# Kernel optimization log

Hardware: AMD Instinct MI355X
Metric: run time of the kernel (lower is better)

The kernel has to match this reference:

```python
import jax, jax.numpy as jnp
import numpy as np

V, D, L, S = 32000, 512, 4096, 256
LOG2 = float(np.log(2.0))


def _self_conflict(a, span):
    # a: [S, l] bool. Sequential: a[i] = a[i] & ~a[i-1] (using updated values).
    def step1(prev, cur):
        out = cur & ~prev
        return out, out
    first = a[:, 0]
    _, rest = jax.lax.scan(step1, first, a[:, 1:].T)  # scan over token axis
    a = jnp.concatenate([first[:, None], rest.T], axis=1)
    if span == 3:
        # second pass: a[i] = a[i] & ~a[i-2] on the updated array
        def step2(carry, cur):
            pm2, pm1 = carry
            out = cur & ~pm2
            return (pm1, out), out
        _, rest2 = jax.lax.scan(step2, (a[:, 0], a[:, 1]), a[:, 2:].T)
        a = jnp.concatenate([a[:, :2], rest2.T], axis=1)
    return a


def _shift_into(a1, off, L2):
    # hit[j] |= a1[j - off], zeros elsewhere
    B, l1 = a1.shape
    out = jnp.zeros((B, L2), dtype=bool)
    if off >= 0:
        end = min(L2, off + l1)
        return out.at[:, off:end].set(a1[:, :end - off])
    return out.at[:, :l1 + off].set(a1[:, -off:])


def _intersec_conflict(a1, a2, flag=False):
    # a2[j] cleared if any overlapping a1 span is active (set of shifts)
    l1, l2 = a1.shape[1], a2.shape[1]
    hit = jnp.zeros_like(a2)
    for i in range(l2 - l1 + 1):
        hit = hit | _shift_into(a1, i, l2)
    if flag:
        hit = hit | _shift_into(a1, -1, l2) | _shift_into(a1, 2, l2)
    return a2 & ~hit


def _forward(x, embd, w1, b1, w2, b2, w3, b3, g1, g2, g3, align1, align2, align3):
    emb = embd[x]                                   # [1, L, D]
    s2 = (emb[:, 1:] + emb[:, :-1]) / 2             # [1, L-1, D]
    s3 = (emb[:, 2:] + emb[:, 1:-1] + emb[:, :-2]) / 3
    heads = ((emb, w1, b1, g1, align1), (s2, w2, b2, g2, align2), (s3, w3, b3, g3, align3))
    stats, bools = [], []
    for spans, w, b, g, amask in heads:
        logits = spans @ w + b                      # [1, l, 2]
        logp = jax.nn.log_softmax(logits, axis=-1)
        p = jnp.exp(logp)
        nent = -(p * logp).sum(-1) / LOG2           # normalized entropy (2 classes)
        idx = jnp.argmax(logp + g, axis=-1)         # [S, l] Gumbel-max categorical sample
        act = jax.nn.one_hot(idx, 2, dtype=logp.dtype)
        bools.append((idx == 0) & amask[None, :])   # reduce chosen AND aligned
        stats.append((logp, nent, act))

    b1_, b2_, b3_ = bools
    b3_ = _self_conflict(b3_, 3)
    b2_ = _intersec_conflict(b3_, b2_, flag=True)
    b1_ = _intersec_conflict(b3_, b1_)
    b2_ = _self_conflict(b2_, 2)
    b1_ = _intersec_conflict(b2_, b1_)

    logp1, ne1, act1 = stats[0]
    logp2, ne2, _ = stats[1]
    logp3, ne3, _ = stats[2]
    # actions 2/3 are rewritten from the conflict-reduced booleans; action 1 keeps its sample
    act2 = jnp.stack([b2_, ~b2_], axis=-1).astype(logp2.dtype)
    act3 = jnp.stack([b3_, ~b3_], axis=-1).astype(logp3.dtype)

    nll1 = -(act1 * logp1).sum(-1).sum(1)           # [S]
    nll2 = -(act2 * logp2).sum(-1).sum(1)
    nll3 = -(act3 * logp3).sum(-1).sum(1)
    nsamp = act1.shape[0]
    nent = jnp.broadcast_to((ne1.mean(1) + ne2.mean(1) + ne3.mean(1)) / 3.0, (nsamp,))
    return nent, nll1 + nll2 + nll3, b1_, b2_, b3_


def setup_inputs():
    key = jax.random.key(0)
    k = jax.random.split(key, 11)
    x = jax.random.randint(k[0], (1, L), 0, V)
    embd = jax.random.normal(k[1], (V, D), jnp.float32) * 0.02
    w1 = jax.random.normal(k[2], (D, 2), jnp.float32) * 0.05
    w2 = jax.random.normal(k[3], (D, 2), jnp.float32) * 0.05
    w3 = jax.random.normal(k[4], (D, 2), jnp.float32) * 0.05
    b1 = jnp.zeros((2,), jnp.float32)
    b2 = jnp.zeros((2,), jnp.float32)
    b3 = jnp.zeros((2,), jnp.float32)
    g1 = jax.random.gumbel(k[5], (S, L, 2), jnp.float32)
    g2 = jax.random.gumbel(k[6], (S, L - 1, 2), jnp.float32)
    g3 = jax.random.gumbel(k[7], (S, L - 2, 2), jnp.float32)
    align1 = jax.random.randint(k[8], (L,), 0, 2).astype(bool)
    align2 = jax.random.randint(k[9], (L - 1,), 0, 2).astype(bool)
    align3 = jax.random.randint(k[10], (L - 2,), 0, 2).astype(bool)
    return {"x": x, "sample_num": S, "align1": align1, "align2": align2, "align3": align3,
            "embd": embd, "w1": w1, "b1": b1, "w2": w2, "b2": b2, "w3": w3, "b3": b3,
            "g1": g1, "g2": g2, "g3": g3}


def reference(x, sample_num, align1, align2, align3, embd, w1, b1, w2, b2, w3, b3, g1, g2, g3):
    return _forward(x, embd, w1, b1, w2, b2, w3, b3, g1, g2, g3, align1, align2, align3)
```

## Files before the change

### kernel.cpp

```cpp
#include <hip/hip_runtime.h>
#include <stdint.h>

#define L_ 4096
#define S_ 256
#define D_ 512
#define NW 64

static __device__ const float LN2F = 0.69314718055994530942f;

__global__ __launch_bounds__(256)
void k_rows(const int* __restrict__ x, const float* __restrict__ embd,
            const float* __restrict__ w1, const float* __restrict__ b1,
            const float* __restrict__ w2, const float* __restrict__ b2,
            const float* __restrict__ w3, const float* __restrict__ b3,
            float* __restrict__ lp, float* __restrict__ entbuf) {
    const int wid  = threadIdx.x >> 6;
    const int lane = threadIdx.x & 63;
    const int t = blockIdx.x * 4 + wid;
    const int t1 = (t + 1 < L_) ? t + 1 : t;
    const int t2 = (t + 2 < L_) ? t + 2 : t;
    const int d0 = lane * 8;

    const float4* e0p = (const float4*)(embd + (size_t)x[t]  * D_ + d0);
    const float4* e1p = (const float4*)(embd + (size_t)x[t1] * D_ + d0);
    const float4* e2p = (const float4*)(embd + (size_t)x[t2] * D_ + d0);
    float4 e0a = e0p[0], e0b = e0p[1];
    float4 e1a = e1p[0], e1b = e1p[1];
    float4 e2a = e2p[0], e2b = e2p[1];
    const float4* w1p = (const float4*)(w1 + 2 * d0);
    const float4* w2p = (const float4*)(w2 + 2 * d0);
    const float4* w3p = (const float4*)(w3 + 2 * d0);

    float v0[8] = {e0a.x,e0a.y,e0a.z,e0a.w,e0b.x,e0b.y,e0b.z,e0b.w};
    float v1[8] = {e1a.x,e1a.y,e1a.z,e1a.w,e1b.x,e1b.y,e1b.z,e1b.w};
    float v2[8] = {e2a.x,e2a.y,e2a.z,e2a.w,e2b.x,e2b.y,e2b.z,e2b.w};
    float wv1[16], wv2[16], wv3[16];
    for (int q = 0; q < 4; q++) {
        float4 a = w1p[q]; wv1[4*q]=a.x; wv1[4*q+1]=a.y; wv1[4*q+2]=a.z; wv1[4*q+3]=a.w;
        float4 b = w2p[q]; wv2[4*q]=b.x; wv2[4*q+1]=b.y; wv2[4*q+2]=b.z; wv2[4*q+3]=b.w;
        float4 c = w3p[q]; wv3[4*q]=c.x; wv3[4*q+1]=c.y; wv3[4*q+2]=c.z; wv3[4*q+3]=c.w;
    }
    double a0=0,a1=0,a2=0,a3=0,a4=0,a5=0;
    #pragma unroll
    for (int j = 0; j < 8; j++) {
        float s2 = (v1[j] + v0[j]) * 0.5f;
        float s3 = ((v2[j] + v1[j]) + v0[j]) / 3.0f;
        a0 += (double)v0[j] * (double)wv1[2*j];
        a1 += (double)v0[j] * (double)wv1[2*j+1];
        a2 += (double)s2    * (double)wv2[2*j];
        a3 += (double)s2    * (double)wv2[2*j+1];
        a4 += (double)s3    * (double)wv3[2*j];
        a5 += (double)s3    * (double)wv3[2*j+1];
    }
    #pragma unroll
    for (int o = 32; o > 0; o >>= 1) {
        a0 += __shfl_xor(a0, o, 64);
        a1 += __shfl_xor(a1, o, 64);
        a2 += __shfl_xor(a2, o, 64);
        a3 += __shfl_xor(a3, o, 64);
        a4 += __shfl_xor(a4, o, 64);
        a5 += __shfl_xor(a5, o, 64);
    }
    if (lane < 3) {
        double l0, l1; const float* bb;
        if (lane == 0)      { l0 = a0; l1 = a1; bb = b1; }
        else if (lane == 1) { l0 = a2; l1 = a3; bb = b2; }
        else                { l0 = a4; l1 = a5; bb = b3; }
        bool valid = (lane == 0) || (lane == 1 && t < L_-1) || (lane == 2 && t < L_-2);
        float ev = 0.0f;
        if (valid) {
            l0 += (double)bb[0]; l1 += (double)bb[1];
            double m = fmax(l0, l1);
            double sa = l0 - m, sb = l1 - m;
            double lse = log(exp(sa) + exp(sb));
            float p0l = (float)(sa - lse), p1l = (float)(sb - lse);
            lp[2*lane*L_ + t] = p0l; lp[(2*lane+1)*L_ + t] = p1l;
            float p0 = expf(p0l), p1 = expf(p1l);
            ev = -(p0*p0l + p1*p1l) / LN2F;
        }
        entbuf[lane*L_ + t] = ev;
    }
}

__device__ __forceinline__ uint64_t pass1_word(uint64_t w, unsigned& carry) {
    uint64_t wp = w & ~(uint64_t)carry;
    uint64_t o = wp & ~(wp << 1);
    uint64_t h = wp & (wp << 1);
    o |= (o << 2)  & h; h &= (h << 2);
    o |= (o << 4)  & h; h &= (h << 4);
    o |= (o << 8)  & h; h &= (h << 8);
    o |= (o << 16) & h; h &= (h << 16);
    o |= (o << 32) & h;
    carry = (unsigned)(o >> 63);
    return o;
}
__device__ __forceinline__ uint64_t pass2_word(uint64_t a, unsigned& qe, unsigned& qo) {
    uint64_t ap = a & ~(uint64_t)qe & ~(((uint64_t)qo) << 1);
    uint64_t o = ap & ~(ap << 2);
    uint64_t h = ap & (ap << 2);
    o |= (o << 4)  & h; h &= (h << 4);
    o |= (o << 8)  & h; h &= (h << 8);
    o |= (o << 16) & h; h &= (h << 16);
    o |= (o << 32) & h;
    qe = (unsigned)((o >> 62) & 1);
    qo = (unsigned)(o >> 63);
    return o;
}

__global__ __launch_bounds__(1024)
void k_fused(const float* __restrict__ lp,
             const int* __restrict__ al1, const int* __restrict__ al2, const int* __restrict__ al3,
             const float2* __restrict__ g1, const float2* __restrict__ g2, const float2* __restrict__ g3,
             float* __restrict__ out) {
    const int s = blockIdx.x;
    const int tid = threadIdx.x;
    const int lane = tid & 63;
    const int wv = tid >> 6;

    __shared__ uint64_t w1s[NW], w2s[NW], w3s[NW];
    __shared__ uint64_t o1s[NW], o2s[NW], o3s[NW];

    float lp2a[4], lp2b[4], lp3a[4], lp3b[4];
    float nllacc = 0.0f;
    #pragma unroll
    for (int it = 0; it < 4; it++) {
        const int t = it * 1024 + tid;
        float2 v1 = g1[(size_t)s * L_ + t];
        float lp0 = lp[t], lp1v = lp[L_ + t];
        bool raw1 = (lp0 + v1.x) >= (lp1v + v1.y);
        bool m1 = raw1 && (al1[t] != 0);
        nllacc += raw1 ? -lp0 : -lp1v;
        bool m2 = false, m3 = false;
        lp2a[it] = 0.f; lp2b[it] = 0.f; lp3a[it] = 0.f; lp3b[it] = 0.f;
        if (t < L_-1) {
            float2 v2 = g2[(size_t)s * (L_-1) + t];
            float a = lp[2*L_+t], b = lp[3*L_+t];
            lp2a[it] = a; lp2b[it] = b;
            m2 = ((a + v2.x) >= (b + v2.y)) && (al2[t] != 0);
        }
        if (t < L_-2) {
            float2 v3 = g3[(size_t)s * (L_-2) + t];
            float a = lp[4*L_+t], b = lp[5*L_+t];
            lp3a[it] = a; lp3b[it] = b;
            m3 = ((a + v3.x) >= (b + v3.y)) && (al3[t] != 0);
        }
        unsigned long long b1b = __ballot(m1);
        unsigned long long b2b = __ballot(m2);
        unsigned long long b3b = __ballot(m3);
        if (lane == 0) {
            int w = t >> 6;
            w1s[w] = b1b; w2s[w] = b2b; w3s[w] = b3b;
        }
    }
    __syncthreads();

    if (tid == 0) {
        unsigned c1 = 0, qe = 0, qo = 0, c2 = 0;
        uint64_t b3m1 = 0, b2m1 = 0;
        uint64_t b3cur = pass2_word(pass1_word(w3s[0], c1), qe, qo);
        for (int j = 0; j < NW; j++) {
            uint64_t b3nx = 0;
            if (j < NW - 1) b3nx = pass2_word(pass1_word(w3s[j+1], c1), qe, qo);
            uint64_t sh1 = (b3cur << 1) | (b3m1 >> 63);
            uint64_t sh2 = (b3cur << 2) | (b3m1 >> 62);
            uint64_t shm = (b3cur >> 1) | (b3nx << 63);
            uint64_t hit2 = b3cur | sh1 | sh2 | shm;
            uint64_t B2 = pass1_word(w2s[j] & ~hit2, c2);
            uint64_t hit1 = b3cur | sh1 | sh2 | B2 | ((B2 << 1) | (b2m1 >> 63));
            uint64_t B1 = w1s[j] & ~hit1;
            o3s[j] = b3cur; o2s[j] = B2; o1s[j] = B1;
            b2m1 = B2; b3m1 = b3cur; b3cur = b3nx;
        }
    }
    __syncthreads();

    float* b1o = out + 2*S_;
    float* b2o = b1o + (size_t)S_ * L_;
    float* b3o = b2o + (size_t)S_ * (L_-1);
    #pragma unroll
    for (int it = 0; it < 4; it++) {
        const int t = it * 1024 + tid;
        const int w = t >> 6, b = t & 63;
        b1o[(size_t)s*L_ + t] = (float)((o1s[w] >> b) & 1);
        if (t < L_-1) {
            unsigned bit = (unsigned)((o2s[w] >> b) & 1);
            b2o[(size_t)s*(L_-1) + t] = (float)bit;
            nllacc += bit ? -lp2a[it] : -lp2b[it];
        }
        if (t < L_-2) {
            unsigned bit = (unsigned)((o3s[w] >> b) & 1);
            b3o[(size_t)s*(L_-2) + t] = (float)bit;
            nllacc += bit ? -lp3a[it] : -lp3b[it];
        }
    }
    #pragma unroll
    for (int o = 32; o > 0; o >>= 1) nllacc += __shfl_xor(nllacc, o, 64);
    __shared__ float red[16];
    if (lane == 0) red[wv] = nllacc;
    __syncthreads();
    if (tid == 0) {
        float tot = 0.f;
        #pragma unroll
        for (int i = 0; i < 16; i++) tot += red[i];
        out[S_ + s] = tot;
    }
}

__global__ __launch_bounds__(256)
void k_nent(const float* __restrict__ entbuf, float* __restrict__ out) {
    const int tid = threadIdx.x;
    double s1 = 0, s2 = 0, s3 = 0;
    for (int t = tid; t < L_; t += 256) {
        s1 += (double)entbuf[t];
        s2 += (double)entbuf[L_ + t];
        s3 += (double)entbuf[2*L_ + t];
    }
    #pragma unroll
    for (int o = 32; o > 0; o >>= 1) {
        s1 += __shfl_xor(s1, o, 64);
        s2 += __shfl_xor(s2, o, 64);
        s3 += __shfl_xor(s3, o, 64);
    }
    __shared__ double red[3][4];
    const int wid = tid >> 6, lane = tid & 63;
    if (lane == 0) { red[0][wid] = s1; red[1][wid] = s2; red[2][wid] = s3; }
    __syncthreads();
    __shared__ float vsh;
    if (tid == 0) {
        double t1 = red[0][0]+red[0][1]+red[0][2]+red[0][3];
        double t2 = red[1][0]+red[1][1]+red[1][2]+red[1][3];
        double t3 = red[2][0]+red[2][1]+red[2][2]+red[2][3];
        vsh = (float)((t1 / (double)L_ + t2 / (double)(L_-1) + t3 / (double)(L_-2)) / 3.0);
    }
    __syncthreads();
    out[tid] = vsh;
}

extern "C" void kernel_launch(void* const* d_in, const int* in_sizes, int n_in,
                              void* d_out, int out_size, void* d_ws, size_t ws_size,
                              hipStream_t stream) {
    const int*   x    = (const int*)d_in[0];
    const int*   al1  = (const int*)d_in[2];
    const int*   al2  = (const int*)d_in[3];
    const int*   al3  = (const int*)d_in[4];
    const float* embd = (const float*)d_in[5];
    const float* w1   = (const float*)d_in[6];
    const float* b1   = (const float*)d_in[7];
    const float* w2   = (const float*)d_in[8];
    const float* b2   = (const float*)d_in[9];
    const float* w3   = (const float*)d_in[10];
    const float* b3   = (const float*)d_in[11];
    const float2* g1  = (const float2*)d_in[12];
    const float2* g2  = (const float2*)d_in[13];
    const float2* g3  = (const float2*)d_in[14];
    float* out = (float*)d_out;

    float* lp     = (float*)d_ws;
    float* entbuf = lp + 6 * L_;

    hipLaunchKernelGGL(k_rows, dim3(1024), dim3(256), 0, stream,
                       x, embd, w1, b1, w2, b2, w3, b3, lp, entbuf);
    hipLaunchKernelGGL(k_fused, dim3(S_), dim3(1024), 0, stream,
                       lp, al1, al2, al3, g1, g2, g3, out);
    hipLaunchKernelGGL(k_nent, dim3(1), dim3(256), 0, stream, entbuf, out);
}
```

Before: 173.2 us.

## Parallelize bitmask conflict resolution with wavefront carry-state scans; fold entropy reduction into fused kernel

The serial single-thread loop over 64 words that propagates carries for the self-conflict and intersection-conflict passes is replaced by a 64-lane wavefront. Each lane computes its word under every possible incoming carry state and combines the state-transition functions with a log-step shuffle scan. This removes a long serial dependency chain on one thread in each block. The separate one-block entropy reduction kernel is also removed: block 0 of the fused kernel does that reduction, saving a kernel launch at the cost of a little extra work in one block.

```diff
diff --git a/kernel.cpp b/kernel.cpp
--- a/kernel.cpp
+++ b/kernel.cpp
@@ -82,8 +82,7 @@
     }
 }
 
-__device__ __forceinline__ uint64_t pass1_word(uint64_t w, unsigned& carry) {
-    uint64_t wp = w & ~(uint64_t)carry;
+__device__ __forceinline__ uint64_t pass1_noc(uint64_t wp) {
     uint64_t o = wp & ~(wp << 1);
     uint64_t h = wp & (wp << 1);
     o |= (o << 2)  & h; h &= (h << 2);
@@ -91,19 +90,15 @@
     o |= (o << 8)  & h; h &= (h << 8);
     o |= (o << 16) & h; h &= (h << 16);
     o |= (o << 32) & h;
-    carry = (unsigned)(o >> 63);
     return o;
 }
-__device__ __forceinline__ uint64_t pass2_word(uint64_t a, unsigned& qe, unsigned& qo) {
-    uint64_t ap = a & ~(uint64_t)qe & ~(((uint64_t)qo) << 1);
+__device__ __forceinline__ uint64_t pass2_noc(uint64_t ap) {
     uint64_t o = ap & ~(ap << 2);
     uint64_t h = ap & (ap << 2);
     o |= (o << 4)  & h; h &= (h << 4);
     o |= (o << 8)  & h; h &= (h << 8);
     o |= (o << 16) & h; h &= (h << 16);
     o |= (o << 32) & h;
-    qe = (unsigned)((o >> 62) & 1);
-    qo = (unsigned)(o >> 63);
     return o;
 }
 
@@ -111,7 +106,7 @@
 void k_fused(const float* __restrict__ lp,
              const int* __restrict__ al1, const int* __restrict__ al2, const int* __restrict__ al3,
              const float2* __restrict__ g1, const float2* __restrict__ g2, const float2* __restrict__ g3,
-             float* __restrict__ out) {
+             const float* __restrict__ entbuf, float* __restrict__ out) {
     const int s = blockIdx.x;
     const int tid = threadIdx.x;
     const int lane = tid & 63;
@@ -154,23 +149,78 @@
     }
     __syncthreads();
 
-    if (tid == 0) {
-        unsigned c1 = 0, qe = 0, qo = 0, c2 = 0;
-        uint64_t b3m1 = 0, b2m1 = 0;
-        uint64_t b3cur = pass2_word(pass1_word(w3s[0], c1), qe, qo);
-        for (int j = 0; j < NW; j++) {
-            uint64_t b3nx = 0;
-            if (j < NW - 1) b3nx = pass2_word(pass1_word(w3s[j+1], c1), qe, qo);
-            uint64_t sh1 = (b3cur << 1) | (b3m1 >> 63);
-            uint64_t sh2 = (b3cur << 2) | (b3m1 >> 62);
-            uint64_t shm = (b3cur >> 1) | (b3nx << 63);
-            uint64_t hit2 = b3cur | sh1 | sh2 | shm;
-            uint64_t B2 = pass1_word(w2s[j] & ~hit2, c2);
-            uint64_t hit1 = b3cur | sh1 | sh2 | B2 | ((B2 << 1) | (b2m1 >> 63));
-            uint64_t B1 = w1s[j] & ~hit1;
-            o3s[j] = b3cur; o2s[j] = B2; o1s[j] = B1;
-            b2m1 = B2; b3m1 = b3cur; b3cur = b3nx;
-        }
+    if (wv == 0) {
+        const int j = lane;
+        uint64_t w3 = w3s[j];
+        uint64_t oA = pass1_noc(w3);
+        uint64_t oB = pass1_noc(w3 & ~1ull);
+        unsigned F = (unsigned)(oA >> 63) | (((unsigned)(oB >> 63)) << 1);
+        #pragma unroll
+        for (int d = 1; d < 64; d <<= 1) {
+            unsigned P = __shfl_up(F, d, 64);
+            if (lane >= d) {
+                unsigned la = P & 1, lb = (P >> 1) & 1;
+                unsigned ra = F & 1, rb = (F >> 1) & 1;
+                F = (la ? rb : ra) | ((lb ? rb : ra) << 1);
+            }
+        }
+        unsigned Fp = __shfl_up(F, 1, 64);
+        unsigned cin = (lane == 0) ? 0u : (Fp & 1);
+        uint64_t p1 = cin ? oB : oA;
+
+        uint64_t q0 = pass2_noc(p1);
+        uint64_t q1 = pass2_noc(p1 & ~1ull);
+        uint64_t q2 = pass2_noc(p1 & ~2ull);
+        uint64_t q3 = pass2_noc(p1 & ~3ull);
+        #define ST_(o) ((unsigned)(((o >> 62) & 1) | (((o >> 63) & 1) << 1)))
+        unsigned G = ST_(q0) | (ST_(q1) << 2) | (ST_(q2) << 4) | (ST_(q3) << 6);
+        #undef ST_
+        #pragma unroll
+        for (int d = 1; d < 64; d <<= 1) {
+            unsigned P = __shfl_up(G, d, 64);
+            if (lane >= d) {
+                unsigned H = 0;
+                #pragma unroll
+                for (int xx = 0; xx < 4; xx++) {
+                    unsigned m = (P >> (2 * xx)) & 3;
+                    H |= ((G >> (2 * m)) & 3) << (2 * xx);
+                }
+                G = H;
+            }
+        }
+        unsigned Gp = __shfl_up(G, 1, 64);
+        unsigned s2in = (lane == 0) ? 0u : (Gp & 3);
+        uint64_t B3 = (s2in == 0) ? q0 : (s2in == 1) ? q1 : (s2in == 2) ? q2 : q3;
+
+        uint64_t B3m1 = __shfl_up((unsigned long long)B3, 1, 64); if (lane == 0)  B3m1 = 0;
+        uint64_t B3nx = __shfl_down((unsigned long long)B3, 1, 64); if (lane == 63) B3nx = 0;
+        uint64_t sh1 = (B3 << 1) | (B3m1 >> 63);
+        uint64_t sh2 = (B3 << 2) | (B3m1 >> 62);
+        uint64_t shm = (B3 >> 1) | (B3nx << 63);
+        uint64_t hit2 = B3 | sh1 | sh2 | shm;
+
+        uint64_t in2 = w2s[j] & ~hit2;
+        uint64_t oA2 = pass1_noc(in2);
+        uint64_t oB2 = pass1_noc(in2 & ~1ull);
+        unsigned F2 = (unsigned)(oA2 >> 63) | (((unsigned)(oB2 >> 63)) << 1);
+        #pragma unroll
+        for (int d = 1; d < 64; d <<= 1) {
+            unsigned P = __shfl_up(F2, d, 64);
+            if (lane >= d) {
+                unsigned la = P & 1, lb = (P >> 1) & 1;
+                unsigned ra = F2 & 1, rb = (F2 >> 1) & 1;
+                F2 = (la ? rb : ra) | ((lb ? rb : ra) << 1);
+            }
+        }
+        unsigned F2p = __shfl_up(F2, 1, 64);
+        unsigned cin2 = (lane == 0) ? 0u : (F2p & 1);
+        uint64_t B2 = cin2 ? oB2 : oA2;
+
+        uint64_t B2m1 = __shfl_up((unsigned long long)B2, 1, 64); if (lane == 0) B2m1 = 0;
+        uint64_t hit1 = B3 | sh1 | sh2 | B2 | ((B2 << 1) | (B2m1 >> 63));
+        uint64_t B1 = w1s[j] & ~hit1;
+
+        o1s[j] = B1; o2s[j] = B2; o3s[j] = B3;
     }
     __syncthreads();
 
@@ -204,36 +254,24 @@
         for (int i = 0; i < 16; i++) tot += red[i];
         out[S_ + s] = tot;
     }
-}
-
-__global__ __launch_bounds__(256)
-void k_nent(const float* __restrict__ entbuf, float* __restrict__ out) {
-    const int tid = threadIdx.x;
-    double s1 = 0, s2 = 0, s3 = 0;
-    for (int t = tid; t < L_; t += 256) {
-        s1 += (double)entbuf[t];
-        s2 += (double)entbuf[L_ + t];
-        s3 += (double)entbuf[2*L_ + t];
-    }
-    #pragma unroll
-    for (int o = 32; o > 0; o >>= 1) {
-        s1 += __shfl_xor(s1, o, 64);
-        s2 += __shfl_xor(s2, o, 64);
-        s3 += __shfl_xor(s3, o, 64);
-    }
-    __shared__ double red[3][4];
-    const int wid = tid >> 6, lane = tid & 63;
-    if (lane == 0) { red[0][wid] = s1; red[1][wid] = s2; red[2][wid] = s3; }
-    __syncthreads();
-    __shared__ float vsh;
-    if (tid == 0) {
-        double t1 = red[0][0]+red[0][1]+red[0][2]+red[0][3];
-        double t2 = red[1][0]+red[1][1]+red[1][2]+red[1][3];
-        double t3 = red[2][0]+red[2][1]+red[2][2]+red[2][3];
-        vsh = (float)((t1 / (double)L_ + t2 / (double)(L_-1) + t3 / (double)(L_-2)) / 3.0);
-    }
-    __syncthreads();
-    out[tid] = vsh;
+
+    if (s == 0 && wv == 0) {
+        double s1 = 0, s2d = 0, s3d = 0;
+        for (int t = lane; t < L_; t += 64) {
+            s1  += (double)entbuf[t];
+            s2d += (double)entbuf[L_ + t];
+            s3d += (double)entbuf[2*L_ + t];
+        }
+        #pragma unroll
+        for (int o = 32; o > 0; o >>= 1) {
+            s1  += __shfl_xor(s1, o, 64);
+            s2d += __shfl_xor(s2d, o, 64);
+            s3d += __shfl_xor(s3d, o, 64);
+        }
+        float v = (float)((s1 / (double)L_ + s2d / (double)(L_-1) + s3d / (double)(L_-2)) / 3.0);
+        #pragma unroll
+        for (int i = 0; i < 4; i++) out[lane + 64*i] = v;
+    }
 }
 
 extern "C" void kernel_launch(void* const* d_in, const int* in_sizes, int n_in,
@@ -261,6 +299,5 @@
     hipLaunchKernelGGL(k_rows, dim3(1024), dim3(256), 0, stream,
                        x, embd, w1, b1, w2, b2, w3, b3, lp, entbuf);
     hipLaunchKernelGGL(k_fused, dim3(S_), dim3(1024), 0, stream,
-                       lp, al1, al2, al3, g1, g2, g3, out);
-    hipLaunchKernelGGL(k_nent, dim3(1), dim3(256), 0, stream, entbuf, out);
-}
+                       lp, al1, al2, al3, g1, g2, g3, entbuf, out);
+}
```

Measured after the change: 168.4 us. 1.03x faster.
